# Optimization experiments

Measured on AMD Instinct MI355X. Metric: run time of the kernel, lower is better.

Reference implementation:

```python
import jax, jax.numpy as jnp
import numpy as np

T, H, NH, NKV, HD = 4096, 2048, 16, 2, 256
ROT = 64           # partial_rotary_factor 0.25 * head_dim 256
HALF = ROT // 2    # 32 == sum(mrope_section [11, 11, 10])
BASE = 10_000_000.0
EPS = 1e-6
SCALE = HD ** -0.5


def setup_inputs() -> dict:
    key = jax.random.key(0)
    ks = jax.random.split(key, 8)
    s = 0.02
    return {
        "positions": jnp.sort(jax.random.randint(ks[0], (3, T), 0, 4096), axis=-1),
        "hidden": jax.random.normal(ks[1], (T, H), jnp.float32),
        "Wq": jax.random.normal(ks[2], (H, NH * HD * 2), jnp.float32) * s,
        "Wk": jax.random.normal(ks[3], (H, NKV * HD), jnp.float32) * s,
        "Wv": jax.random.normal(ks[4], (H, NKV * HD), jnp.float32) * s,
        "Wo": jax.random.normal(ks[5], (NH * HD, H), jnp.float32) * s,
        "q_norm_w": jax.random.normal(ks[6], (HD,), jnp.float32) * 0.1,
        "k_norm_w": jax.random.normal(ks[7], (HD,), jnp.float32) * 0.1,
    }


def _rms(x, w):
    # GemmaRMSNorm: x / rms * (1 + w), per-head over last dim
    var = jnp.mean(x * x, axis=-1, keepdims=True)
    return x * jax.lax.rsqrt(var + EPS) * (1.0 + w)


def _rope_tables(positions):
    # interleaved MRoPE: freq j uses position axis j % 3 -> counts [11,11,10]
    inv_freq = BASE ** (-jnp.arange(0, ROT, 2, dtype=jnp.float32) / ROT)  # [HALF]
    axis = jnp.arange(HALF) % 3
    pos = positions[axis, :].astype(jnp.float32)   # [HALF, T]
    freqs = pos.T * inv_freq                       # [T, HALF]
    return jnp.cos(freqs), jnp.sin(freqs)


def _apply_rope(x, cos, sin):
    # x: [T, heads, HD]; rotate first ROT dims (neox half-split), rest pass through
    x1, x2 = x[..., :HALF], x[..., HALF:ROT]
    c, s = cos[:, None, :], sin[:, None, :]
    return jnp.concatenate([x1 * c - x2 * s, x2 * c + x1 * s, x[..., ROT:]], axis=-1)


def reference(positions, hidden, Wq, Wk, Wv, Wo, q_norm_w, k_norm_w):
    qg = (hidden @ Wq).reshape(T, NH, 2 * HD)
    q, gate = qg[..., :HD], qg[..., HD:]          # chunk(2, dim=-1)
    k = (hidden @ Wk).reshape(T, NKV, HD)
    v = (hidden @ Wv).reshape(T, NKV, HD)
    q = _rms(q, q_norm_w)
    k = _rms(k, k_norm_w)
    cos, sin = _rope_tables(positions)
    q = _apply_rope(q, cos, sin)
    k = _apply_rope(k, cos, sin)
    # GQA causal attention: group 16 Q heads over 2 KV heads
    g = NH // NKV
    q4 = q.reshape(T, NKV, g, HD)
    scores = jnp.einsum('qkgd,tkd->kgqt', q4, k) * SCALE   # [NKV, g, T, T]
    mask = jnp.tril(jnp.ones((T, T), dtype=bool))
    scores = jnp.where(mask[None, None], scores, -jnp.inf)
    probs = jax.nn.softmax(scores, axis=-1)
    o = jnp.einsum('kgqt,tkd->qkgd', probs, v).reshape(T, NH, HD)
    o = o * jax.nn.sigmoid(gate)                   # per-head output gating
    return o.reshape(T, NH * HD) @ Wo
```

## Files before the change

kernel.cpp:

```cpp
#include <hip/hip_runtime.h>
#include <hip/hip_bf16.h>


#define T_SZ 4096
#define H_SZ 2048
#define NH_SZ 16
#define NKV_SZ 2
#define HD_SZ 256
#define ATT_SCALE 0.0625f
#define SOFT_M 18.0f
#define EPS_ 1e-6f

typedef __attribute__((ext_vector_type(8))) short bf16x8;
typedef __attribute__((ext_vector_type(4))) float f32x4;

#define MFMA16(a, b, c) __builtin_amdgcn_mfma_f32_16x16x32_bf16((a), (b), (c), 0, 0, 0)

__device__ __forceinline__ void async16(const void* g, void* l) {
  __builtin_amdgcn_global_load_lds((const __attribute__((address_space(1))) void*)g,
                                   (__attribute__((address_space(3))) void*)l,
                                   16, 0, 0);
}

__device__ __forceinline__ float to_f(float x) { return x; }
__device__ __forceinline__ float to_f(__hip_bfloat16 x) { return __bfloat162float(x); }

union BfBits { __hip_bfloat16 h; unsigned short u; };

__device__ __forceinline__ unsigned short bf16_bits(__hip_bfloat16 h) {
  BfBits t; t.h = h; return t.u;
}

__device__ __forceinline__ unsigned pack_hilo(float v) {
  __hip_bfloat16 hi = __float2bfloat16(v);
  float rem = v - __bfloat162float(hi);
  __hip_bfloat16 lo = __float2bfloat16(rem);
  return (unsigned)bf16_bits(hi) | ((unsigned)bf16_bits(lo) << 16);
}

__global__ __launch_bounds__(256) void cast_f32_bf16(const float* __restrict__ in,
                                                     __hip_bfloat16* __restrict__ out,
                                                     int n4) {
  int i = blockIdx.x * 256 + threadIdx.x;
  if (i >= n4) return;
  float4 v = ((const float4*)in)[i];
  union { __hip_bfloat16 h[4]; uint2 u; } t;
  t.h[0] = __float2bfloat16(v.x);
  t.h[1] = __float2bfloat16(v.y);
  t.h[2] = __float2bfloat16(v.z);
  t.h[3] = __float2bfloat16(v.w);
  ((uint2*)out)[i] = t.u;
}

template <typename TIN>
__global__ __launch_bounds__(256) void transpose_cast(const TIN* __restrict__ in,
                                                      __hip_bfloat16* __restrict__ out,
                                                      int R, int C) {
  __shared__ TIN tile[32][33];
  int c0 = blockIdx.x * 32, r0 = blockIdx.y * 32;
  int tx = threadIdx.x & 31, ty = threadIdx.x >> 5;
#pragma unroll
  for (int i = 0; i < 32; i += 8)
    tile[ty + i][tx] = in[(long)(r0 + ty + i) * C + c0 + tx];
  __syncthreads();
#pragma unroll
  for (int i = 0; i < 32; i += 8)
    out[(long)(c0 + ty + i) * R + r0 + tx] = __float2bfloat16(to_f(tile[tx][ty + i]));
}

template <int OUTF32>
__global__ __launch_bounds__(256) void gemm_bt(const __hip_bfloat16* __restrict__ A,
                                               const __hip_bfloat16* __restrict__ BT,
                                               void* __restrict__ Cp,
                                               int M, int N, int K) {
  __shared__ __align__(16) __hip_bfloat16 As[128 * 32];
  __shared__ __align__(16) __hip_bfloat16 Bs[128 * 32];
  const int tid = threadIdx.x;
  const int wid = tid >> 6, lane = tid & 63;
  const int lo = lane & 15, quad = lane >> 4;
  const long m0 = (long)blockIdx.y * 128, n0 = (long)blockIdx.x * 128;
  const int wm = (wid >> 1) * 64, wn = (wid & 1) * 64;
  const f32x4 z4 = {0.f, 0.f, 0.f, 0.f};
  f32x4 acc[4][4];
#pragma unroll
  for (int i = 0; i < 4; ++i)
#pragma unroll
    for (int j = 0; j < 4; ++j) acc[i][j] = z4;

  const int cf0 = tid, cf1 = 256 + tid;
  const int r0_ = cf0 >> 2, c0_ = (cf0 & 3) * 8;
  const int r1_ = cf1 >> 2, c1_ = (cf1 & 3) * 8;
  const __hip_bfloat16* a0 = A + (m0 + r0_) * K + c0_;
  const __hip_bfloat16* a1 = A + (m0 + r1_) * K + c1_;
  const __hip_bfloat16* b0 = BT + (n0 + r0_) * K + c0_;
  const __hip_bfloat16* b1 = BT + (n0 + r1_) * K + c1_;

  for (int k0 = 0; k0 < K; k0 += 32) {
    async16(a0 + k0, As + cf0 * 8);
    async16(a1 + k0, As + cf1 * 8);
    async16(b0 + k0, Bs + cf0 * 8);
    async16(b1 + k0, Bs + cf1 * 8);
    __syncthreads();
    bf16x8 af[4], bfv[4];
#pragma unroll
    for (int i = 0; i < 4; ++i)
      af[i] = *(const bf16x8*)(As + (wm + i * 16 + lo) * 32 + quad * 8);
#pragma unroll
    for (int i = 0; i < 4; ++i)
      bfv[i] = *(const bf16x8*)(Bs + (wn + i * 16 + lo) * 32 + quad * 8);
#pragma unroll
    for (int i = 0; i < 4; ++i)
#pragma unroll
      for (int j = 0; j < 4; ++j) acc[i][j] = MFMA16(af[i], bfv[j], acc[i][j]);
    __syncthreads();
  }
#pragma unroll
  for (int i = 0; i < 4; ++i)
#pragma unroll
    for (int j = 0; j < 4; ++j)
#pragma unroll
      for (int r = 0; r < 4; ++r) {
        long row = m0 + wm + i * 16 + quad * 4 + r;
        long col = n0 + wn + j * 16 + lo;
        float v = acc[i][j][r];
        if (OUTF32)
          ((float*)Cp)[row * N + col] = v;
        else
          ((__hip_bfloat16*)Cp)[row * N + col] = __float2bfloat16(v);
      }
}

__global__ __launch_bounds__(256) void gemm_qg(const __hip_bfloat16* __restrict__ A,
                                               const __hip_bfloat16* __restrict__ BT,
                                               float* __restrict__ qout,
                                               __hip_bfloat16* __restrict__ gate,
                                               int M, int N, int K) {
  __shared__ __align__(16) __hip_bfloat16 As[128 * 32];
  __shared__ __align__(16) __hip_bfloat16 Bs[128 * 32];
  const int tid = threadIdx.x;
  const int wid = tid >> 6, lane = tid & 63;
  const int lo = lane & 15, quad = lane >> 4;
  const long m0 = (long)blockIdx.y * 128, n0 = (long)blockIdx.x * 128;
  const int wm = (wid >> 1) * 64, wn = (wid & 1) * 64;
  const f32x4 z4 = {0.f, 0.f, 0.f, 0.f};
  f32x4 acc[4][4];
#pragma unroll
  for (int i = 0; i < 4; ++i)
#pragma unroll
    for (int j = 0; j < 4; ++j) acc[i][j] = z4;

  const int cf0 = tid, cf1 = 256 + tid;
  const int r0_ = cf0 >> 2, c0_ = (cf0 & 3) * 8;
  const int r1_ = cf1 >> 2, c1_ = (cf1 & 3) * 8;
  const __hip_bfloat16* a0 = A + (m0 + r0_) * K + c0_;
  const __hip_bfloat16* a1 = A + (m0 + r1_) * K + c1_;
  const __hip_bfloat16* b0 = BT + (n0 + r0_) * K + c0_;
  const __hip_bfloat16* b1 = BT + (n0 + r1_) * K + c1_;

  for (int k0 = 0; k0 < K; k0 += 32) {
    async16(a0 + k0, As + cf0 * 8);
    async16(a1 + k0, As + cf1 * 8);
    async16(b0 + k0, Bs + cf0 * 8);
    async16(b1 + k0, Bs + cf1 * 8);
    __syncthreads();
    bf16x8 af[4], bfv[4];
#pragma unroll
    for (int i = 0; i < 4; ++i)
      af[i] = *(const bf16x8*)(As + (wm + i * 16 + lo) * 32 + quad * 8);
#pragma unroll
    for (int i = 0; i < 4; ++i)
      bfv[i] = *(const bf16x8*)(Bs + (wn + i * 16 + lo) * 32 + quad * 8);
#pragma unroll
    for (int i = 0; i < 4; ++i)
#pragma unroll
      for (int j = 0; j < 4; ++j) acc[i][j] = MFMA16(af[i], bfv[j], acc[i][j]);
    __syncthreads();
  }
#pragma unroll
  for (int i = 0; i < 4; ++i)
#pragma unroll
    for (int j = 0; j < 4; ++j)
#pragma unroll
      for (int r = 0; r < 4; ++r) {
        long row = m0 + wm + i * 16 + quad * 4 + r;
        long col = n0 + wn + j * 16 + lo;
        int head = (int)(col >> 9), c = (int)(col & 511);
        float v = acc[i][j][r];
        if (c < 256)
          qout[(row * NH_SZ + head) * 256 + c] = v;
        else
          gate[(row * NH_SZ + head) * 256 + (c - 256)] = __float2bfloat16(v);
      }
}

__global__ __launch_bounds__(256) void v_swizzle(const __hip_bfloat16* __restrict__ vraw,
                                                 __hip_bfloat16* __restrict__ vsw) {
  const int ktt = blockIdx.x, kvh = blockIdx.y, tid = threadIdx.x;
  __shared__ __hip_bfloat16 L[64 * 264];
#pragma unroll
  for (int it = 0; it < 8; ++it) {
    int cf = it * 256 + tid;
    int kv = cf >> 5, d0 = (cf & 31) * 8;
    *(uint4*)&L[kv * 264 + d0] =
        *(const uint4*)&vraw[(((long)ktt * 64 + kv) * NKV_SZ + kvh) * 256 + d0];
  }
  __syncthreads();
#pragma unroll
  for (int it = 0; it < 8; ++it) {
    int cf = it * 256 + tid;
    int c = cf >> 8, d = cf & 255;
    union { __hip_bfloat16 h[8]; uint4 u; } t;
#pragma unroll
    for (int e = 0; e < 8; ++e) t.h[e] = L[(c * 8 + e) * 264 + d];
    *(uint4*)&vsw[((long)kvh * 64 + ktt) * 16384 + (long)(c * 256 + d) * 8] = t.u;
  }
}

__global__ __launch_bounds__(256) void norm_rope_pack(float* __restrict__ qbuf,
                                                      const float* __restrict__ kbuf,
                                                      __hip_bfloat16* __restrict__ ksw,
                                                      const int* __restrict__ pos,
                                                      const float* __restrict__ qw,
                                                      const float* __restrict__ kw) {
  const int t = blockIdx.x, h = blockIdx.y, d = threadIdx.x;
  __shared__ float buf[256];
  __shared__ float red[4];
  const float* ptr;
  const float* w;
  if (h < NH_SZ) {
    ptr = qbuf + ((long)t * NH_SZ + h) * 256;
    w = qw;
  } else {
    ptr = kbuf + ((long)t * NKV_SZ + (h - NH_SZ)) * 256;
    w = kw;
  }
  float x = ptr[d];
  float s2 = x * x;
#pragma unroll
  for (int o = 32; o > 0; o >>= 1) s2 += __shfl_down(s2, o);
  if ((d & 63) == 0) red[d >> 6] = s2;
  __syncthreads();
  float tot = red[0] + red[1] + red[2] + red[3];
  float sc = rsqrtf(tot * (1.0f / 256.0f) + EPS_);
  buf[d] = x * sc * (1.0f + w[d]);
  __syncthreads();
  float outv;
  if (d < 64) {
    int i = d & 31;
    float p = (float)pos[(i % 3) * T_SZ + t];
    float fr = p * exp2f((float)i * (-0.72667177075661f));
    float c, s;
    sincosf(fr, &s, &c);
    if (d < 32)
      outv = buf[d] * c - buf[d + 32] * s;
    else
      outv = buf[d] * c + buf[d - 32] * s;
  } else {
    outv = buf[d];
  }
  if (h < NH_SZ) {
    ((unsigned*)qbuf)[((long)t * NH_SZ + h) * 256 + d] = pack_hilo(outv);
  } else {
    int kv = h - NH_SZ;
    long tt = t >> 5, r = t & 31;
    int c = d >> 3, e = d & 7;
    ksw[(((long)kv * 128 + tt) * 32 + c) * 256 + r * 8 + e] = __float2bfloat16(outv);
  }
}

__global__ __launch_bounds__(256) void attn_kernel(unsigned* __restrict__ Qp,
                                                   const __hip_bfloat16* __restrict__ Ksw,
                                                   const __hip_bfloat16* __restrict__ Vsw,
                                                   const __hip_bfloat16* __restrict__ Gt) {
  const int w = blockIdx.x + blockIdx.y * 64;
  const int xcd = w & 7, j = w >> 3;
  const int h = xcd * 2 + (j & 1);
  const int qt = 63 - (j >> 1);
  const int kvh = h >> 3;
  const int tid = threadIdx.x, wid = tid >> 6, lane = tid & 63;
  const int lo = lane & 15, quad = lane >> 4;
  __shared__ __align__(16) __hip_bfloat16 Ks[32 * 256];
  __shared__ __align__(16) __hip_bfloat16 Vs[4 * 2048];
  __shared__ __align__(16) __hip_bfloat16 Ps[4][16 * 40];

  __hip_bfloat16* myP = &Ps[wid][0];
  const f32x4 z4 = {0.f, 0.f, 0.f, 0.f};
  const int nt = 2 * (qt + 1);

  bf16x8 qh[8], ql[8];
  {
    const unsigned* qp =
        Qp + ((long)(qt * 64 + wid * 16 + lo) * NH_SZ + h) * 256 + quad * 8;
#pragma unroll
    for (int kc = 0; kc < 8; ++kc) {
      uint4 p0 = *(const uint4*)(qp + kc * 32);
      uint4 p1 = *(const uint4*)(qp + kc * 32 + 4);
      bf16x8 a, b;
      a[0] = (short)(p0.x & 0xffff); b[0] = (short)(p0.x >> 16);
      a[1] = (short)(p0.y & 0xffff); b[1] = (short)(p0.y >> 16);
      a[2] = (short)(p0.z & 0xffff); b[2] = (short)(p0.z >> 16);
      a[3] = (short)(p0.w & 0xffff); b[3] = (short)(p0.w >> 16);
      a[4] = (short)(p1.x & 0xffff); b[4] = (short)(p1.x >> 16);
      a[5] = (short)(p1.y & 0xffff); b[5] = (short)(p1.y >> 16);
      a[6] = (short)(p1.z & 0xffff); b[6] = (short)(p1.z >> 16);
      a[7] = (short)(p1.w & 0xffff); b[7] = (short)(p1.w >> 16);
      qh[kc] = a; ql[kc] = b;
    }
  }

  f32x4 acc[16];
#pragma unroll
  for (int od = 0; od < 16; ++od) acc[od] = z4;
  float lsum[4];
#pragma unroll
  for (int r = 0; r < 4; ++r) lsum[r] = 0.f;

  const int qrow_g = qt * 64 + wid * 16 + quad * 4;
  const __hip_bfloat16* kbase = Ksw + (long)kvh * 1048576;
  const __hip_bfloat16* vbase = Vsw + (long)kvh * 1048576;

#pragma unroll
  for (int i = 0; i < 4; ++i) {
    int m = i * 4 + wid;
    async16(kbase + m * 512 + lane * 8, Ks + m * 512 + lane * 8);
    async16(vbase + m * 512 + lane * 8, Vs + m * 512 + lane * 8);
  }
  __syncthreads();

  for (int kt = 0; kt < nt; ++kt) {
    const bool skip = (kt == nt - 1) && (wid < 2);
    f32x4 s[2];
    s[0] = z4; s[1] = z4;
    if (!skip) {
      __builtin_amdgcn_s_setprio(1);
#pragma unroll
      for (int kc = 0; kc < 8; ++kc) {
        bf16x8 ah = qh[kc], al = ql[kc];
#pragma unroll
        for (int ni = 0; ni < 2; ++ni) {
          bf16x8 b = *(const bf16x8*)(Ks + (kc * 4 + quad) * 256 + (ni * 16 + lo) * 8);
          s[ni] = MFMA16(ah, b, s[ni]);
          s[ni] = MFMA16(al, b, s[ni]);
        }
      }
      __builtin_amdgcn_s_setprio(0);
    }
    __syncthreads();
    if (kt + 1 < nt) {
      const __hip_bfloat16* kb = kbase + (long)(kt + 1) * 8192;
#pragma unroll
      for (int i = 0; i < 4; ++i) {
        int m = i * 4 + wid;
        async16(kb + m * 512 + lane * 8, Ks + m * 512 + lane * 8);
      }
    }
    if (!skip) {
      float sv[2][4];
      if (kt >= nt - 2) {
#pragma unroll
        for (int ni = 0; ni < 2; ++ni) {
          int kcol = kt * 32 + ni * 16 + lo;
#pragma unroll
          for (int r = 0; r < 4; ++r) {
            float e = __expf(fmaf(s[ni][r], ATT_SCALE, -SOFT_M));
            sv[ni][r] = (kcol > qrow_g + r) ? 0.f : e;
          }
        }
      } else {
#pragma unroll
        for (int ni = 0; ni < 2; ++ni)
#pragma unroll
          for (int r = 0; r < 4; ++r)
            sv[ni][r] = __expf(fmaf(s[ni][r], ATT_SCALE, -SOFT_M));
      }
#pragma unroll
      for (int r = 0; r < 4; ++r) lsum[r] += sv[0][r] + sv[1][r];
#pragma unroll
      for (int ni = 0; ni < 2; ++ni)
#pragma unroll
        for (int r = 0; r < 4; ++r)
          myP[(quad * 4 + r) * 40 + ni * 16 + lo] = __float2bfloat16(sv[ni][r]);
      bf16x8 ap = *(const bf16x8*)(myP + lo * 40 + quad * 8);
      __builtin_amdgcn_s_setprio(1);
#pragma unroll
      for (int od = 0; od < 16; ++od) {
        bf16x8 bv = *(const bf16x8*)(Vs + quad * 2048 + (od * 16 + lo) * 8);
        acc[od] = MFMA16(ap, bv, acc[od]);
      }
      __builtin_amdgcn_s_setprio(0);
    }
    __syncthreads();
    if (kt + 1 < nt) {
      const __hip_bfloat16* vb = vbase + (long)(kt + 1) * 8192;
#pragma unroll
      for (int i = 0; i < 4; ++i) {
        int m = i * 4 + wid;
        async16(vb + m * 512 + lane * 8, Vs + m * 512 + lane * 8);
      }
    }
  }

  float l_r[4];
#pragma unroll
  for (int r = 0; r < 4; ++r) {
    float su = lsum[r];
#pragma unroll
    for (int off = 1; off < 16; off <<= 1) su += __shfl_xor(su, off);
    l_r[r] = su;
  }
#pragma unroll
  for (int od = 0; od < 16; ++od)
#pragma unroll
    for (int r = 0; r < 4; ++r) {
      int trow = qt * 64 + wid * 16 + quad * 4 + r;
      int col = od * 16 + lo;
      long idx = ((long)trow * NH_SZ + h) * 256 + col;
      float g = __bfloat162float(Gt[idx]);
      float sig = 1.0f / (1.0f + expf(-g));
      float v = (acc[od][r] / l_r[r]) * sig;
      Qp[idx] = pack_hilo(v);
    }
}

__global__ __launch_bounds__(256) void gemm_out(const unsigned* __restrict__ Ap,
                                                const __hip_bfloat16* __restrict__ Bt,
                                                float* __restrict__ C,
                                                int M, int N, int K) {
  __shared__ __align__(16) __hip_bfloat16 Ash[128 * 32];
  __shared__ __align__(16) __hip_bfloat16 Asl[128 * 32];
  __shared__ __align__(16) __hip_bfloat16 Bs[128 * 32];
  const int tid = threadIdx.x;
  const int wid = tid >> 6, lane = tid & 63;
  const int lo = lane & 15, quad = lane >> 4;
  const long m0 = (long)blockIdx.y * 128, n0 = (long)blockIdx.x * 128;
  const int wm = (wid >> 1) * 64, wn = (wid & 1) * 64;
  const f32x4 z4 = {0.f, 0.f, 0.f, 0.f};
  f32x4 acc[4][4];
#pragma unroll
  for (int i = 0; i < 4; ++i)
#pragma unroll
    for (int j = 0; j < 4; ++j) acc[i][j] = z4;

  const int cf0 = tid, cf1 = 256 + tid;
  const int br0 = cf0 >> 2, bc0 = (cf0 & 3) * 8;
  const int br1 = cf1 >> 2, bc1 = (cf1 & 3) * 8;
  const __hip_bfloat16* b0 = Bt + (n0 + br0) * K + bc0;
  const __hip_bfloat16* b1 = Bt + (n0 + br1) * K + bc1;

  for (int k0 = 0; k0 < K; k0 += 32) {
    async16(b0 + k0, Bs + cf0 * 8);
    async16(b1 + k0, Bs + cf1 * 8);
#pragma unroll
    for (int it = 0; it < 4; ++it) {
      int c = it * 256 + tid, row = c >> 3, c4 = (c & 7) * 4;
      uint4 p = *(const uint4*)(Ap + (m0 + row) * K + k0 + c4);
      uint2 wh, wl;
      wh.x = (p.x & 0xffff) | ((p.y & 0xffff) << 16);
      wh.y = (p.z & 0xffff) | ((p.w & 0xffff) << 16);
      wl.x = (p.x >> 16) | (p.y & 0xffff0000u);
      wl.y = (p.z >> 16) | (p.w & 0xffff0000u);
      *(uint2*)(Ash + row * 32 + c4) = wh;
      *(uint2*)(Asl + row * 32 + c4) = wl;
    }
    __syncthreads();
    bf16x8 ah[4], al[4], bf[4];
#pragma unroll
    for (int i = 0; i < 4; ++i) {
      ah[i] = *(const bf16x8*)(Ash + (wm + i * 16 + lo) * 32 + quad * 8);
      al[i] = *(const bf16x8*)(Asl + (wm + i * 16 + lo) * 32 + quad * 8);
      bf[i] = *(const bf16x8*)(Bs + (wn + i * 16 + lo) * 32 + quad * 8);
    }
#pragma unroll
    for (int i = 0; i < 4; ++i)
#pragma unroll
      for (int j = 0; j < 4; ++j) {
        acc[i][j] = MFMA16(ah[i], bf[j], acc[i][j]);
        acc[i][j] = MFMA16(al[i], bf[j], acc[i][j]);
      }
    __syncthreads();
  }
#pragma unroll
  for (int i = 0; i < 4; ++i)
#pragma unroll
    for (int j = 0; j < 4; ++j)
#pragma unroll
      for (int r = 0; r < 4; ++r) {
        long row = m0 + wm + i * 16 + quad * 4 + r;
        long col = n0 + wn + j * 16 + lo;
        C[row * N + col] = acc[i][j][r];
      }
}

extern "C" void kernel_launch(void* const* d_in, const int* in_sizes, int n_in,
                              void* d_out, int out_size, void* d_ws, size_t ws_size,
                              hipStream_t stream) {
  (void)in_sizes; (void)n_in; (void)out_size; (void)ws_size;
  const int* positions = (const int*)d_in[0];
  const float* hidden = (const float*)d_in[1];
  const float* Wq = (const float*)d_in[2];
  const float* Wk = (const float*)d_in[3];
  const float* Wv = (const float*)d_in[4];
  const float* Wo = (const float*)d_in[5];
  const float* qw = (const float*)d_in[6];
  const float* kw = (const float*)d_in[7];
  float* out = (float*)d_out;
  char* ws = (char*)d_ws;

  __hip_bfloat16* hid  = (__hip_bfloat16*)(ws + 0);
  __hip_bfloat16* WqT  = (__hip_bfloat16*)(ws + 16777216);
  __hip_bfloat16* WkT  = (__hip_bfloat16*)(ws + 50331648);
  __hip_bfloat16* WvT  = (__hip_bfloat16*)(ws + 52428800);
  float*          qf   = (float*)(ws + 54525952);
  __hip_bfloat16* gate = (__hip_bfloat16*)(ws + 121634816);
  float*          kf   = (float*)(ws + 155189248);
  __hip_bfloat16* vraw = (__hip_bfloat16*)(ws + 163577856);
  __hip_bfloat16* Ksw  = WkT;
  __hip_bfloat16* Vsw  = hid;
  __hip_bfloat16* WoT  = gate;
  unsigned* qpk = (unsigned*)qf;

  cast_f32_bf16<<<dim3(8192), dim3(256), 0, stream>>>(hidden, hid, 2097152);
  transpose_cast<float><<<dim3(256, 64), dim3(256), 0, stream>>>(Wq, WqT, 2048, 8192);
  transpose_cast<float><<<dim3(16, 64), dim3(256), 0, stream>>>(Wk, WkT, 2048, 512);
  transpose_cast<float><<<dim3(16, 64), dim3(256), 0, stream>>>(Wv, WvT, 2048, 512);
  gemm_qg<<<dim3(64, 32), dim3(256), 0, stream>>>(hid, WqT, qf, gate, 4096, 8192, 2048);
  gemm_bt<1><<<dim3(4, 32), dim3(256), 0, stream>>>(hid, WkT, kf, 4096, 512, 2048);
  gemm_bt<0><<<dim3(4, 32), dim3(256), 0, stream>>>(hid, WvT, vraw, 4096, 512, 2048);
  v_swizzle<<<dim3(64, 2), dim3(256), 0, stream>>>(vraw, Vsw);
  norm_rope_pack<<<dim3(4096, 18), dim3(256), 0, stream>>>(qf, kf, Ksw, positions, qw, kw);
  attn_kernel<<<dim3(64, 16), dim3(256), 0, stream>>>(qpk, Ksw, Vsw, gate);
  transpose_cast<float><<<dim3(64, 128), dim3(256), 0, stream>>>(Wo, WoT, 4096, 2048);
  gemm_out<<<dim3(16, 32), dim3(256), 0, stream>>>(qpk, WoT, out, 4096, 2048, 4096);
}
```

Baseline: 888.3 us.

## Fuse K/V projections, remap GEMM tiles per XCD, wave-level norm+rope

Replaces the two separate K and V projection GEMMs with one GEMM over the contiguous WkT/WvT buffer. Its epilogue splits output columns into fp32 K and bf16 V. Block indices in the Q/gate and output GEMMs are remapped so each XCD works on a contiguous group of N tiles, aiming for better L2 reuse of B tiles. The norm+rope kernel now uses one wavefront per (token, head) with float4 loads, shuffle-only reductions and vectorized stores, which removes shared memory and block barriers. The fused GEMM depends on WvT sitting directly after WkT in the workspace.

New measurement: 903.5 us. About the same (+1.7%).

```diff
diff --git a/kernel.cpp b/kernel.cpp
--- a/kernel.cpp
+++ b/kernel.cpp
@@ -68,68 +68,6 @@
     out[(long)(c0 + ty + i) * R + r0 + tx] = __float2bfloat16(to_f(tile[tx][ty + i]));
 }
 
-template <int OUTF32>
-__global__ __launch_bounds__(256) void gemm_bt(const __hip_bfloat16* __restrict__ A,
-                                               const __hip_bfloat16* __restrict__ BT,
-                                               void* __restrict__ Cp,
-                                               int M, int N, int K) {
-  __shared__ __align__(16) __hip_bfloat16 As[128 * 32];
-  __shared__ __align__(16) __hip_bfloat16 Bs[128 * 32];
-  const int tid = threadIdx.x;
-  const int wid = tid >> 6, lane = tid & 63;
-  const int lo = lane & 15, quad = lane >> 4;
-  const long m0 = (long)blockIdx.y * 128, n0 = (long)blockIdx.x * 128;
-  const int wm = (wid >> 1) * 64, wn = (wid & 1) * 64;
-  const f32x4 z4 = {0.f, 0.f, 0.f, 0.f};
-  f32x4 acc[4][4];
-#pragma unroll
-  for (int i = 0; i < 4; ++i)
-#pragma unroll
-    for (int j = 0; j < 4; ++j) acc[i][j] = z4;
-
-  const int cf0 = tid, cf1 = 256 + tid;
-  const int r0_ = cf0 >> 2, c0_ = (cf0 & 3) * 8;
-  const int r1_ = cf1 >> 2, c1_ = (cf1 & 3) * 8;
-  const __hip_bfloat16* a0 = A + (m0 + r0_) * K + c0_;
-  const __hip_bfloat16* a1 = A + (m0 + r1_) * K + c1_;
-  const __hip_bfloat16* b0 = BT + (n0 + r0_) * K + c0_;
-  const __hip_bfloat16* b1 = BT + (n0 + r1_) * K + c1_;
-
-  for (int k0 = 0; k0 < K; k0 += 32) {
-    async16(a0 + k0, As + cf0 * 8);
-    async16(a1 + k0, As + cf1 * 8);
-    async16(b0 + k0, Bs + cf0 * 8);
-    async16(b1 + k0, Bs + cf1 * 8);
-    __syncthreads();
-    bf16x8 af[4], bfv[4];
-#pragma unroll
-    for (int i = 0; i < 4; ++i)
-      af[i] = *(const bf16x8*)(As + (wm + i * 16 + lo) * 32 + quad * 8);
-#pragma unroll
-    for (int i = 0; i < 4; ++i)
-      bfv[i] = *(const bf16x8*)(Bs + (wn + i * 16 + lo) * 32 + quad * 8);
-#pragma unroll
-    for (int i = 0; i < 4; ++i)
-#pragma unroll
-      for (int j = 0; j < 4; ++j) acc[i][j] = MFMA16(af[i], bfv[j], acc[i][j]);
-    __syncthreads();
-  }
-#pragma unroll
-  for (int i = 0; i < 4; ++i)
-#pragma unroll
-    for (int j = 0; j < 4; ++j)
-#pragma unroll
-      for (int r = 0; r < 4; ++r) {
-        long row = m0 + wm + i * 16 + quad * 4 + r;
-        long col = n0 + wn + j * 16 + lo;
-        float v = acc[i][j][r];
-        if (OUTF32)
-          ((float*)Cp)[row * N + col] = v;
-        else
-          ((__hip_bfloat16*)Cp)[row * N + col] = __float2bfloat16(v);
-      }
-}
-
 __global__ __launch_bounds__(256) void gemm_qg(const __hip_bfloat16* __restrict__ A,
                                                const __hip_bfloat16* __restrict__ BT,
                                                float* __restrict__ qout,
@@ -140,7 +78,10 @@
   const int tid = threadIdx.x;
   const int wid = tid >> 6, lane = tid & 63;
   const int lo = lane & 15, quad = lane >> 4;
-  const long m0 = (long)blockIdx.y * 128, n0 = (long)blockIdx.x * 128;
+  const int wq = blockIdx.x + blockIdx.y * 64;
+  const int xcd = wq & 7, idx = wq >> 3;
+  const long n0 = (long)(xcd * 8 + (idx & 7)) * 128;
+  const long m0 = (long)(idx >> 3) * 128;
   const int wm = (wid >> 1) * 64, wn = (wid & 1) * 64;
   const f32x4 z4 = {0.f, 0.f, 0.f, 0.f};
   f32x4 acc[4][4];
@@ -193,6 +134,71 @@
       }
 }
 
+__global__ __launch_bounds__(256) void gemm_kv(const __hip_bfloat16* __restrict__ A,
+                                               const __hip_bfloat16* __restrict__ BT,
+                                               float* __restrict__ kf,
+                                               __hip_bfloat16* __restrict__ vraw,
+                                               int M, int N, int K) {
+  __shared__ __align__(16) __hip_bfloat16 As[128 * 32];
+  __shared__ __align__(16) __hip_bfloat16 Bs[128 * 32];
+  const int tid = threadIdx.x;
+  const int wid = tid >> 6, lane = tid & 63;
+  const int lo = lane & 15, quad = lane >> 4;
+  const int wq = blockIdx.x + blockIdx.y * 8;
+  const int xcd = wq & 7, idx = wq >> 3;
+  const long n0 = (long)xcd * 128;
+  const long m0 = (long)idx * 128;
+  const int wm = (wid >> 1) * 64, wn = (wid & 1) * 64;
+  const f32x4 z4 = {0.f, 0.f, 0.f, 0.f};
+  f32x4 acc[4][4];
+#pragma unroll
+  for (int i = 0; i < 4; ++i)
+#pragma unroll
+    for (int j = 0; j < 4; ++j) acc[i][j] = z4;
+
+  const int cf0 = tid, cf1 = 256 + tid;
+  const int r0_ = cf0 >> 2, c0_ = (cf0 & 3) * 8;
+  const int r1_ = cf1 >> 2, c1_ = (cf1 & 3) * 8;
+  const __hip_bfloat16* a0 = A + (m0 + r0_) * K + c0_;
+  const __hip_bfloat16* a1 = A + (m0 + r1_) * K + c1_;
+  const __hip_bfloat16* b0 = BT + (n0 + r0_) * K + c0_;
+  const __hip_bfloat16* b1 = BT + (n0 + r1_) * K + c1_;
+
+  for (int k0 = 0; k0 < K; k0 += 32) {
+    async16(a0 + k0, As + cf0 * 8);
+    async16(a1 + k0, As + cf1 * 8);
+    async16(b0 + k0, Bs + cf0 * 8);
+    async16(b1 + k0, Bs + cf1 * 8);
+    __syncthreads();
+    bf16x8 af[4], bfv[4];
+#pragma unroll
+    for (int i = 0; i < 4; ++i)
+      af[i] = *(const bf16x8*)(As + (wm + i * 16 + lo) * 32 + quad * 8);
+#pragma unroll
+    for (int i = 0; i < 4; ++i)
+      bfv[i] = *(const bf16x8*)(Bs + (wn + i * 16 + lo) * 32 + quad * 8);
+#pragma unroll
+    for (int i = 0; i < 4; ++i)
+#pragma unroll
+      for (int j = 0; j < 4; ++j) acc[i][j] = MFMA16(af[i], bfv[j], acc[i][j]);
+    __syncthreads();
+  }
+#pragma unroll
+  for (int i = 0; i < 4; ++i)
+#pragma unroll
+    for (int j = 0; j < 4; ++j)
+#pragma unroll
+      for (int r = 0; r < 4; ++r) {
+        long row = m0 + wm + i * 16 + quad * 4 + r;
+        long col = n0 + wn + j * 16 + lo;
+        float v = acc[i][j][r];
+        if (col < 512)
+          kf[row * 512 + col] = v;
+        else
+          vraw[row * 512 + (col - 512)] = __float2bfloat16(v);
+      }
+}
+
 __global__ __launch_bounds__(256) void v_swizzle(const __hip_bfloat16* __restrict__ vraw,
                                                  __hip_bfloat16* __restrict__ vsw) {
   const int ktt = blockIdx.x, kvh = blockIdx.y, tid = threadIdx.x;
@@ -216,55 +222,62 @@
   }
 }
 
-__global__ __launch_bounds__(256) void norm_rope_pack(float* __restrict__ qbuf,
+__global__ __launch_bounds__(256) void norm_rope_wave(float* __restrict__ qbuf,
                                                       const float* __restrict__ kbuf,
                                                       __hip_bfloat16* __restrict__ ksw,
                                                       const int* __restrict__ pos,
                                                       const float* __restrict__ qw,
                                                       const float* __restrict__ kw) {
-  const int t = blockIdx.x, h = blockIdx.y, d = threadIdx.x;
-  __shared__ float buf[256];
-  __shared__ float red[4];
-  const float* ptr;
-  const float* w;
-  if (h < NH_SZ) {
-    ptr = qbuf + ((long)t * NH_SZ + h) * 256;
-    w = qw;
+  const int id = blockIdx.x * 4 + (threadIdx.x >> 6);
+  const int lane = threadIdx.x & 63;
+  const int h = id % 18, t = id / 18;
+  const bool isq = h < NH_SZ;
+  const float* ptr = isq ? qbuf + ((long)t * NH_SZ + h) * 256
+                         : kbuf + ((long)t * NKV_SZ + (h - NH_SZ)) * 256;
+  const float* w = isq ? qw : kw;
+  float4 v = *(const float4*)(ptr + lane * 4);
+  float4 wv = *(const float4*)(w + lane * 4);
+  float s2 = v.x * v.x + v.y * v.y + v.z * v.z + v.w * v.w;
+#pragma unroll
+  for (int o = 32; o > 0; o >>= 1) s2 += __shfl_xor(s2, o);
+  float sc = rsqrtf(s2 * (1.0f / 256.0f) + EPS_);
+  float n[4];
+  n[0] = v.x * sc * (1.0f + wv.x);
+  n[1] = v.y * sc * (1.0f + wv.y);
+  n[2] = v.z * sc * (1.0f + wv.z);
+  n[3] = v.w * sc * (1.0f + wv.w);
+  float pr[4];
+#pragma unroll
+  for (int j = 0; j < 4; ++j) pr[j] = __shfl_xor(n[j], 8);
+  float o4[4];
+  if (lane < 16) {
+    int base_i = (lane & 7) * 4;
+#pragma unroll
+    for (int j = 0; j < 4; ++j) {
+      int i = base_i + j;
+      float p = (float)pos[(i % 3) * T_SZ + t];
+      float fr = p * exp2f((float)i * (-0.72667177075661f));
+      float c, s;
+      sincosf(fr, &s, &c);
+      o4[j] = (lane < 8) ? n[j] * c - pr[j] * s : n[j] * c + pr[j] * s;
+    }
   } else {
-    ptr = kbuf + ((long)t * NKV_SZ + (h - NH_SZ)) * 256;
-    w = kw;
-  }
-  float x = ptr[d];
-  float s2 = x * x;
-#pragma unroll
-  for (int o = 32; o > 0; o >>= 1) s2 += __shfl_down(s2, o);
-  if ((d & 63) == 0) red[d >> 6] = s2;
-  __syncthreads();
-  float tot = red[0] + red[1] + red[2] + red[3];
-  float sc = rsqrtf(tot * (1.0f / 256.0f) + EPS_);
-  buf[d] = x * sc * (1.0f + w[d]);
-  __syncthreads();
-  float outv;
-  if (d < 64) {
-    int i = d & 31;
-    float p = (float)pos[(i % 3) * T_SZ + t];
-    float fr = p * exp2f((float)i * (-0.72667177075661f));
-    float c, s;
-    sincosf(fr, &s, &c);
-    if (d < 32)
-      outv = buf[d] * c - buf[d + 32] * s;
-    else
-      outv = buf[d] * c + buf[d - 32] * s;
-  } else {
-    outv = buf[d];
-  }
-  if (h < NH_SZ) {
-    ((unsigned*)qbuf)[((long)t * NH_SZ + h) * 256 + d] = pack_hilo(outv);
+#pragma unroll
+    for (int j = 0; j < 4; ++j) o4[j] = n[j];
+  }
+  if (isq) {
+    uint4 u;
+    u.x = pack_hilo(o4[0]); u.y = pack_hilo(o4[1]);
+    u.z = pack_hilo(o4[2]); u.w = pack_hilo(o4[3]);
+    *(uint4*)((unsigned*)qbuf + ((long)t * NH_SZ + h) * 256 + lane * 4) = u;
   } else {
     int kv = h - NH_SZ;
-    long tt = t >> 5, r = t & 31;
-    int c = d >> 3, e = d & 7;
-    ksw[(((long)kv * 128 + tt) * 32 + c) * 256 + r * 8 + e] = __float2bfloat16(outv);
+    long tt = t >> 5; int r = t & 31;
+    int c = lane >> 1, e0 = (lane & 1) * 4;
+    union { __hip_bfloat16 h4[4]; uint2 u; } kk;
+#pragma unroll
+    for (int j = 0; j < 4; ++j) kk.h4[j] = __float2bfloat16(o4[j]);
+    *(uint2*)&ksw[(((long)kv * 128 + tt) * 32 + c) * 256 + r * 8 + e0] = kk.u;
   }
 }
 
@@ -432,7 +445,10 @@
   const int tid = threadIdx.x;
   const int wid = tid >> 6, lane = tid & 63;
   const int lo = lane & 15, quad = lane >> 4;
-  const long m0 = (long)blockIdx.y * 128, n0 = (long)blockIdx.x * 128;
+  const int wq = blockIdx.x + blockIdx.y * 16;
+  const int xcd = wq & 7, idx = wq >> 3;
+  const long n0 = (long)(xcd * 2 + (idx & 1)) * 128;
+  const long m0 = (long)(idx >> 1) * 128;
   const int wm = (wid >> 1) * 64, wn = (wid & 1) * 64;
   const f32x4 z4 = {0.f, 0.f, 0.f, 0.f};
   f32x4 acc[4][4];
@@ -524,10 +540,9 @@
   transpose_cast<float><<<dim3(16, 64), dim3(256), 0, stream>>>(Wk, WkT, 2048, 512);
   transpose_cast<float><<<dim3(16, 64), dim3(256), 0, stream>>>(Wv, WvT, 2048, 512);
   gemm_qg<<<dim3(64, 32), dim3(256), 0, stream>>>(hid, WqT, qf, gate, 4096, 8192, 2048);
-  gemm_bt<1><<<dim3(4, 32), dim3(256), 0, stream>>>(hid, WkT, kf, 4096, 512, 2048);
-  gemm_bt<0><<<dim3(4, 32), dim3(256), 0, stream>>>(hid, WvT, vraw, 4096, 512, 2048);
+  gemm_kv<<<dim3(8, 32), dim3(256), 0, stream>>>(hid, WkT, kf, vraw, 4096, 1024, 2048);
   v_swizzle<<<dim3(64, 2), dim3(256), 0, stream>>>(vraw, Vsw);
-  norm_rope_pack<<<dim3(4096, 18), dim3(256), 0, stream>>>(qf, kf, Ksw, positions, qw, kw);
+  norm_rope_wave<<<dim3(18432), dim3(256), 0, stream>>>(qf, kf, Ksw, positions, qw, kw);
   attn_kernel<<<dim3(64, 16), dim3(256), 0, stream>>>(qpk, Ksw, Vsw, gate);
   transpose_cast<float><<<dim3(64, 128), dim3(256), 0, stream>>>(Wo, WoT, 4096, 2048);
   gemm_out<<<dim3(16, 32), dim3(256), 0, stream>>>(qpk, WoT, out, 4096, 2048, 4096);
```
